# Kernel tuning notes

Hardware: AMD Instinct MI355X
Metric: run time of the kernel (lower is better)

Reference implementation:

```python
import jax, jax.numpy as jnp
import numpy as np

B, C, H, W = 4, 256, 64, 64
CP = C // 4  # embedding_channels, k=4 hardcoded
# branch index -> (key-stream i, query/value-stream j); streams: 0=t,1=b,2=m
IIDX = np.array([0, 0, 0, 1, 1, 1, 2, 2, 2])  # which stream feeds k
JIDX = np.array([0, 1, 2, 0, 1, 2, 0, 1, 2])  # which stream feeds q and v


def setup_inputs() -> dict:
    key = jax.random.key(0)
    ks = jax.random.split(key, 6)
    scale = 0.05
    return {
        "t": jax.random.normal(ks[0], (B, C, H, W), jnp.float32),
        "b": jax.random.normal(ks[1], (B, C, H, W), jnp.float32),
        "m": jax.random.normal(ks[2], (B, C, H, W), jnp.float32),
        "W_qkv": jax.random.normal(ks[3], (9, C, C), jnp.float32) * scale,
        "W_red": jax.random.normal(ks[4], (9, CP, C), jnp.float32) * scale,
        "W_rec": jax.random.normal(ks[5], (9, C, CP), jnp.float32) * scale,
    }


def _pool(x):
    # ChannelAttention: global avg pool + global max pool -> [B, C']
    return jnp.mean(x, axis=(2, 3)) + jnp.max(x, axis=(2, 3))


def _channel_attention(q, k, v, w_red, w_rec):
    # q,k,v: [B,C,H,W]; w_red: [C',C]; w_rec: [C,C']
    ori = q + k + v
    red = lambda x: jax.nn.relu(jnp.einsum("bchw,ec->behw", x, w_red))
    qr, kr, vr = red(q), red(k), red(v)
    f = _pool(kr)  # key   -> [B,C']
    g = _pool(qr)  # query -> [B,C']
    h = _pool(vr)  # value -> [B,C']
    # s = f^T g : [B,C',C']; softmax over dim=1 (rows), per torch nn.Softmax(dim=1)
    s = f[:, :, None] * g[:, None, :]
    beta = jax.nn.softmax(s, axis=1)
    vout = jnp.einsum("bi,bij->bj", h, beta)  # [B,C']
    # recovery 1x1 conv on [B,C',1,1]; bilinear upsample from 1x1 == broadcast
    o = jax.nn.sigmoid(jnp.einsum("be,ce->bc", vout, w_rec))  # [B,C]
    return o[:, :, None, None] * ori


def reference(t, b, m, W_qkv, W_red, W_rec):
    x = jnp.stack([t, b, m])  # [3,B,C,H,W]
    Wp = W_qkv.reshape(3, 3, C, C)  # [stream, (q,k,v), C_out, C_in]
    proj = jnp.einsum("sbchw,sjec->sjbehw", x, Wp)  # [3,3,B,C,H,W]
    Q, K, V = proj[:, 0], proj[:, 1], proj[:, 2]  # each [3,B,C,H,W]
    q9, k9, v9 = Q[JIDX], K[IIDX], V[JIDX]  # [9,B,C,H,W]
    outs = jax.vmap(_channel_attention)(q9, k9, v9, W_red, W_rec)
    return outs.sum(axis=0)
```

## Files before the change

### kernel.cpp

```cpp
#include <hip/hip_runtime.h>

#define Bn 4
#define Cn 256
#define HWn 4096
#define CPn 64
#define MP 640

typedef unsigned short u16;
typedef unsigned int u32;

using short8  = __attribute__((ext_vector_type(8))) short;
using floatx4 = __attribute__((ext_vector_type(4))) float;

static __device__ __forceinline__ u16 f2bf(float f) {
    union { float f; u32 u; } v; v.f = f;
    u32 r = (v.u + 0x7FFFu + ((v.u >> 16) & 1u)) >> 16;
    return (u16)r;
}

static __device__ __forceinline__ void gld16(const u16* g, u16* l) {
    __builtin_amdgcn_global_load_lds(
        (const __attribute__((address_space(1))) u32*)g,
        (__attribute__((address_space(3))) u32*)l, 16, 0, 0);
}


__global__ __launch_bounds__(256) void prep(
    const float* __restrict__ Tt, const float* __restrict__ Bt, const float* __restrict__ Mt,
    const float* __restrict__ Wqkv, const float* __restrict__ Wred,
    u16* __restrict__ xT, u16* __restrict__ CWp)
{
    __shared__ u16 T[64][72];
    __shared__ float As[16][64];
    __shared__ float Bs[16][64];
    const int t = threadIdx.x;

    if (blockIdx.z < 3) {
        const int s  = blockIdx.z, b = blockIdx.y;
        const int ct = blockIdx.x & 3, hwt = blockIdx.x >> 2;
        const int c0 = ct * 64, hw0 = hwt * 64;
        const float* X = (s == 0 ? Tt : (s == 1 ? Bt : Mt)) + (size_t)b * Cn * HWn;

        const int cl = t >> 2, q = t & 3;
        const float* src = X + (size_t)(c0 + cl) * HWn + hw0 + q * 16;
        #pragma unroll
        for (int u = 0; u < 4; ++u) {
            const float4 v = *(const float4*)(src + u * 4);
            T[cl][q * 16 + u * 4 + 0] = f2bf(v.x);
            T[cl][q * 16 + u * 4 + 1] = f2bf(v.y);
            T[cl][q * 16 + u * 4 + 2] = f2bf(v.z);
            T[cl][q * 16 + u * 4 + 3] = f2bf(v.w);
        }
        __syncthreads();

        const int wl = t >> 2;
        u16* dst = xT + ((size_t)((s * Bn + b) * HWn) + hw0 + wl) * Cn + c0 + q * 16;
        #pragma unroll
        for (int u = 0; u < 2; ++u) {
            u32 w0 = (u32)T[q * 16 + u * 8 + 0][wl] | ((u32)T[q * 16 + u * 8 + 1][wl] << 16);
            u32 w1 = (u32)T[q * 16 + u * 8 + 2][wl] | ((u32)T[q * 16 + u * 8 + 3][wl] << 16);
            u32 w2 = (u32)T[q * 16 + u * 8 + 4][wl] | ((u32)T[q * 16 + u * 8 + 5][wl] << 16);
            u32 w3 = (u32)T[q * 16 + u * 8 + 6][wl] | ((u32)T[q * 16 + u * 8 + 7][wl] << 16);
            uint4 pk = {w0, w1, w2, w3};
            *(uint4*)(dst + u * 8) = pk;
        }
        return;
    }

    const int lin = blockIdx.y * 256 + blockIdx.x;
    if (lin >= 108) return;
    const int c0  = (lin & 3) * 64;
    const int rest = lin >> 2;
    const int y9 = rest % 9, s = rest / 9;
    const int tt = y9 / 3, m3 = y9 % 3;
    const int idx = (tt == 1) ? (3 * s + m3) : (3 * m3 + s);

    const float* A  = Wred + (size_t)idx * CPn * Cn;
    const float* Bm = Wqkv + (size_t)(3 * s + tt) * Cn * Cn;

    const int ty = t >> 4, tx = t & 15;
    float acc[4][4] = {};

    for (int k0 = 0; k0 < Cn; k0 += 16) {
        {
            const int r = t >> 2, eq = (t & 3) * 4;
            const float4 a = *(const float4*)(A + (size_t)r * Cn + k0 + eq);
            As[eq + 0][r] = a.x; As[eq + 1][r] = a.y; As[eq + 2][r] = a.z; As[eq + 3][r] = a.w;
        }
        {
            const int r = t >> 4, cq = (t & 15) * 4;
            *(float4*)(&Bs[r][cq]) = *(const float4*)(Bm + (size_t)(k0 + r) * Cn + c0 + cq);
        }
        __syncthreads();
        #pragma unroll
        for (int k = 0; k < 16; ++k) {
            const float4 a4 = *(const float4*)(&As[k][ty * 4]);
            const float4 b4 = *(const float4*)(&Bs[k][tx * 4]);
            const float a[4] = {a4.x, a4.y, a4.z, a4.w};
            const float bb[4] = {b4.x, b4.y, b4.z, b4.w};
            #pragma unroll
            for (int i = 0; i < 4; ++i)
                #pragma unroll
                for (int j = 0; j < 4; ++j)
                    acc[i][j] = fmaf(a[i], bb[j], acc[i][j]);
        }
        __syncthreads();
    }

    u16* outp = CWp + (size_t)s * MP * Cn;
    #pragma unroll
    for (int i = 0; i < 4; ++i) {
        const int row = tt * 192 + m3 * 64 + ty * 4 + i;
        unsigned long long pk =
            (unsigned long long)f2bf(acc[i][0]) |
            ((unsigned long long)f2bf(acc[i][1]) << 16) |
            ((unsigned long long)f2bf(acc[i][2]) << 32) |
            ((unsigned long long)f2bf(acc[i][3]) << 48);
        *(unsigned long long*)(outp + (size_t)row * Cn + c0 + tx * 4) = pk;
    }
}

#define NSUB 16

__global__ __launch_bounds__(256, 1) void redpool_mfma(
    const u16* __restrict__ xT, const u16* __restrict__ CWp,
    float* __restrict__ Psum, float* __restrict__ Pmax)
{
    const int s   = blockIdx.z;
    const int mt  = blockIdx.x >> 4, nch = blockIdx.x & 15;
    const int m0  = mt * 128;
    const int nbase = nch * 1024;

    const u16* Ap = CWp + (size_t)s * MP * Cn;
    const u16* Bp = xT + (size_t)s * Bn * HWn * Cn;

    __shared__ __align__(16) u16 Bs[2][32 * 512];

    const int t = threadIdx.x;
    const int w = t >> 6, lane = t & 63;
    const int l15 = lane & 15, q = lane >> 4;
    const int wr = w >> 1, wc = w & 1;

    short8 af[4][8];
    {
        const u16* Arow = Ap + (size_t)(m0 + wr * 64 + l15) * Cn + q * 8;
        #pragma unroll
        for (int i = 0; i < 4; ++i)
            #pragma unroll
            for (int kk = 0; kk < 8; ++kk)
                af[i][kk] = *(const short8*)(Arow + (size_t)(i * 16) * Cn + kk * 32);
    }

    auto stageB = [&](int it, int buf) {
        const u16* Bsrc = Bp + (size_t)(nbase + it * 64 + l15) * Cn + q * 8;
        #pragma unroll
        for (int pi = 0; pi < 8; ++pi) {
            const int p = w * 8 + pi;
            gld16(Bsrc + (size_t)((p >> 3) * 16) * Cn + (p & 7) * 32, &Bs[buf][p * 512]);
        }
    };
    stageB(0, 0);

    float rs[4][4] = {};
    float rm[4][4] = {};

    for (int it = 0; it < NSUB; ++it) {
        __syncthreads();
        if (it + 1 < NSUB) stageB(it + 1, (it + 1) & 1);
        const u16* bb = Bs[it & 1];

        floatx4 acc[4][2] = {};
        #pragma unroll
        for (int kk = 0; kk < 8; ++kk) {
            short8 bf[2];
            #pragma unroll
            for (int j = 0; j < 2; ++j)
                bf[j] = *(const short8*)&bb[((wc * 2 + j) * 8 + kk) * 512 + lane * 8];
            #pragma unroll
            for (int i = 0; i < 4; ++i)
                #pragma unroll
                for (int j = 0; j < 2; ++j)
                    acc[i][j] = __builtin_amdgcn_mfma_f32_16x16x32_bf16(af[i][kk], bf[j], acc[i][j], 0, 0, 0);
        }
        #pragma unroll
        for (int i = 0; i < 4; ++i)
            #pragma unroll
            for (int r = 0; r < 4; ++r) {
                const float v0 = fmaxf(acc[i][0][r], 0.f);
                const float v1 = fmaxf(acc[i][1][r], 0.f);
                rs[i][r] += v0 + v1;
                rm[i][r] = fmaxf(rm[i][r], fmaxf(v0, v1));
            }
    }

    #pragma unroll
    for (int i = 0; i < 4; ++i)
        #pragma unroll
        for (int r = 0; r < 4; ++r) {
            #pragma unroll
            for (int off = 1; off < 16; off <<= 1) {
                rs[i][r] += __shfl_xor(rs[i][r], off);
                rm[i][r] = fmaxf(rm[i][r], __shfl_xor(rm[i][r], off));
            }
        }

    __syncthreads();
    float* Lsum = (float*)&Bs[0][0];
    float* Lmax = Lsum + 256;
    if (l15 == 0) {
        #pragma unroll
        for (int i = 0; i < 4; ++i)
            #pragma unroll
            for (int r = 0; r < 4; ++r) {
                const int row = wr * 64 + i * 16 + q * 4 + r;
                Lsum[wc * 128 + row] = rs[i][r];
                Lmax[wc * 128 + row] = rm[i][r];
            }
    }
    __syncthreads();
    if (t < 128) {
        const int R = m0 + t;
        const size_t o = ((size_t)s * MP + R) * 16 + nch;
        Psum[o] = Lsum[t] + Lsum[128 + t];
        Pmax[o] = fmaxf(Lmax[t], Lmax[128 + t]);
    }
}

__global__ __launch_bounds__(64) void attn_small(
    const float* __restrict__ Psum, const float* __restrict__ Pmax,
    float* __restrict__ vout)
{
    const int idx = blockIdx.x / Bn;
    const int bb  = blockIdx.x % Bn;
    __shared__ float ff[CPn], gg[CPn], hh[CPn];
    const int t = threadIdx.x;

    float v[3];
    #pragma unroll
    for (int tt = 0; tt < 3; ++tt) {
        const int s_ = (tt == 1) ? idx / 3 : idx % 3;
        const int m3 = (tt == 1) ? idx % 3 : idx / 3;
        const int R  = tt * 192 + m3 * 64 + t;
        const size_t base = ((size_t)s_ * MP + R) * 16 + bb * 4;
        float sm = 0.f, mx = 0.f;
        #pragma unroll
        for (int u = 0; u < 4; ++u) {
            sm += Psum[base + u];
            mx = fmaxf(mx, Pmax[base + u]);
        }
        v[tt] = sm * (1.0f / HWn) + mx;
    }
    gg[t] = v[0];
    ff[t] = v[1];
    hh[t] = v[2];
    __syncthreads();

    const float gj = gg[t];
    float mx = -1e30f;
    for (int i = 0; i < CPn; ++i) mx = fmaxf(mx, ff[i] * gj);
    float den = 0.f, num = 0.f;
    for (int i = 0; i < CPn; ++i) {
        const float e = expf(ff[i] * gj - mx);
        den += e;
        num += hh[i] * e;
    }
    vout[((size_t)idx * Bn + bb) * CPn + t] = num / den;
}

__global__ __launch_bounds__(256) void build_M(
    const float* __restrict__ Wqkv, const float* __restrict__ Wrec,
    const float* __restrict__ vout, u16* __restrict__ Mm)
{
    const int s = blockIdx.x >> 8, m = blockIdx.x & 255;
    const int b = blockIdx.y;
    const int t = threadIdx.x;
    __shared__ float cc[2];

    if (t < CPn) {
        float d[6];
        #pragma unroll
        for (int j = 0; j < 6; ++j) {
            const int idx = (j < 3) ? (s + 3 * j) : (3 * s + (j - 3));
            d[j] = vout[((size_t)idx * Bn + b) * CPn + t] *
                   Wrec[((size_t)idx * Cn + m) * CPn + t];
        }
        #pragma unroll
        for (int off = 32; off >= 1; off >>= 1)
            #pragma unroll
            for (int j = 0; j < 6; ++j)
                d[j] += __shfl_xor(d[j], off);
        if (t == 0) {
            float cA = 0.f, cK = 0.f;
            #pragma unroll
            for (int j = 0; j < 3; ++j) {
                cA += 1.0f / (1.0f + expf(-d[j]));
                cK += 1.0f / (1.0f + expf(-d[j + 3]));
            }
            cc[0] = cA; cc[1] = cK;
        }
    }
    __syncthreads();
    const float cA = cc[0], cK = cc[1];
    const float wq = Wqkv[((size_t)(3 * s + 0) * Cn + m) * Cn + t];
    const float wk = Wqkv[((size_t)(3 * s + 1) * Cn + m) * Cn + t];
    const float wv = Wqkv[((size_t)(3 * s + 2) * Cn + m) * Cn + t];
    Mm[((size_t)(b * 256 + m)) * 768 + s * 256 + t] = f2bf(cA * (wq + wv) + cK * wk);
}

__global__ __launch_bounds__(256, 1) void final_mfma(
    const u16* __restrict__ xT, const u16* __restrict__ Mm,
    float* __restrict__ out)
{
    const int b  = blockIdx.y;
    const int mt = blockIdx.x >> 5, nt = blockIdx.x & 31;
    const int m0 = mt * 128, n0 = nt * 128;

    __shared__ __align__(16) u16 As[2][32 * 512];
    __shared__ __align__(16) u16 Bs[2][32 * 512];

    const int t = threadIdx.x;
    const int w = t >> 6, lane = t & 63;
    const int l15 = lane & 15, q = lane >> 4;
    const int rb = (w >> 1) * 64, cb = (w & 1) * 64;

    auto stage = [&](int it, int buf) {
        const int k0 = it * 128;
        const int s = k0 >> 8, c0 = k0 & 255;
        const u16* Asrc = Mm + (size_t)(b * 256 + m0 + l15) * 768 + k0 + q * 8;
        const u16* Bsrc = xT + ((size_t)((s * Bn + b) * HWn) + n0 + l15) * Cn + c0 + q * 8;
        #pragma unroll
        for (int pi = 0; pi < 8; ++pi) {
            const int p = w * 8 + pi;
            const size_t roff = (size_t)((p >> 2) * 16);
            gld16(Asrc + roff * 768 + (p & 3) * 32, &As[buf][p * 512]);
            gld16(Bsrc + roff * Cn + (p & 3) * 32, &Bs[buf][p * 512]);
        }
    };
    stage(0, 0);

    floatx4 acc[4][4] = {};

    for (int it = 0; it < 6; ++it) {
        __syncthreads();
        if (it + 1 < 6) stage(it + 1, (it + 1) & 1);
        const u16* as = As[it & 1];
        const u16* bs = Bs[it & 1];
        #pragma unroll
        for (int kk = 0; kk < 4; ++kk) {
            short8 af[4], bf[4];
            #pragma unroll
            for (int i = 0; i < 4; ++i)
                af[i] = *(const short8*)&as[((((w >> 1) * 4 + i) << 2) + kk) * 512 + lane * 8];
            #pragma unroll
            for (int j = 0; j < 4; ++j)
                bf[j] = *(const short8*)&bs[((((w & 1) * 4 + j) << 2) + kk) * 512 + lane * 8];
            #pragma unroll
            for (int i = 0; i < 4; ++i)
                #pragma unroll
                for (int j = 0; j < 4; ++j)
                    acc[i][j] = __builtin_amdgcn_mfma_f32_16x16x32_bf16(af[i], bf[j], acc[i][j], 0, 0, 0);
        }
    }

    #pragma unroll
    for (int i = 0; i < 4; ++i)
        #pragma unroll
        for (int j = 0; j < 4; ++j)
            #pragma unroll
            for (int r = 0; r < 4; ++r) {
                const int row = m0 + rb + i * 16 + q * 4 + r;
                const int col = n0 + cb + j * 16 + l15;
                out[((size_t)(b * 256) + row) * HWn + col] = acc[i][j][r];
            }
}

extern "C" void kernel_launch(void* const* d_in, const int* in_sizes, int n_in,
                              void* d_out, int out_size, void* d_ws, size_t ws_size,
                              hipStream_t stream)
{
    const float* Tt   = (const float*)d_in[0];
    const float* Bt   = (const float*)d_in[1];
    const float* Mt   = (const float*)d_in[2];
    const float* Wqkv = (const float*)d_in[3];
    const float* Wred = (const float*)d_in[4];
    const float* Wrec = (const float*)d_in[5];
    float* out = (float*)d_out;

    unsigned char* p = (unsigned char*)d_ws;
    u16* xT = (u16*)p;            p += (size_t)3 * Bn * HWn * Cn * 2;
    u16* Mm = (u16*)p;            p += (size_t)Bn * 256 * 768 * 2;
    u16* CWp = (u16*)p;           p += (size_t)3 * MP * Cn * 2;
    float* Psum = (float*)p;      p += (size_t)3 * MP * 16 * 4;
    float* Pmax = (float*)p;      p += (size_t)3 * MP * 16 * 4;
    float* vout = (float*)p;      p += (size_t)9 * Bn * CPn * 4;

    prep        <<<dim3(256, Bn, 4), 256, 0, stream>>>(Tt, Bt, Mt, Wqkv, Wred, xT, CWp);
    redpool_mfma<<<dim3(80, 1, 3),   256, 0, stream>>>(xT, CWp, Psum, Pmax);
    attn_small  <<<9 * Bn,            64, 0, stream>>>(Psum, Pmax, vout);
    build_M     <<<dim3(768, Bn),    256, 0, stream>>>(Wqkv, Wrec, vout, Mm);
    final_mfma  <<<dim3(64, Bn),     256, 0, stream>>>(xT, Mm, out);
}
```

Before: 168.5 us.

## Fuse all stages into one persistent kernel with software grid barriers

Replaces five separate kernel launches with one persistent 256-block kernel. The prep, reduction-pool, attention, M-build and final GEMM phases are separated by atomic-counter grid barriers, and the counters are cleared with a memset beforehand. This removes launch gaps and inter-kernel drain, but limits parallelism to 256 blocks per phase. It also adds spin-wait barrier overhead and s_setprio hints around the MFMA loop, and correctness relies on all blocks being co-resident.

After: 258.9 us. 1.54x slower.

```diff
diff --git a/kernel.cpp b/kernel.cpp
--- a/kernel.cpp
+++ b/kernel.cpp
@@ -8,6 +8,7 @@
 
 typedef unsigned short u16;
 typedef unsigned int u32;
+typedef unsigned long long u64;
 
 using short8  = __attribute__((ext_vector_type(8))) short;
 using floatx4 = __attribute__((ext_vector_type(4))) float;
@@ -24,354 +25,352 @@
         (__attribute__((address_space(3))) u32*)l, 16, 0, 0);
 }
 
-
-__global__ __launch_bounds__(256) void prep(
+__global__ __launch_bounds__(256, 1) void mega(
     const float* __restrict__ Tt, const float* __restrict__ Bt, const float* __restrict__ Mt,
-    const float* __restrict__ Wqkv, const float* __restrict__ Wred,
-    u16* __restrict__ xT, u16* __restrict__ CWp)
+    const float* __restrict__ Wqkv, const float* __restrict__ Wred, const float* __restrict__ Wrec,
+    u16* __restrict__ xT, u16* __restrict__ CWp,
+    float* __restrict__ Psum, float* __restrict__ Pmax,
+    float* __restrict__ vout, u16* __restrict__ Mm,
+    float* __restrict__ out, u32* __restrict__ gcnt)
 {
-    __shared__ u16 T[64][72];
-    __shared__ float As[16][64];
-    __shared__ float Bs[16][64];
-    const int t = threadIdx.x;
-
-    if (blockIdx.z < 3) {
-        const int s  = blockIdx.z, b = blockIdx.y;
-        const int ct = blockIdx.x & 3, hwt = blockIdx.x >> 2;
-        const int c0 = ct * 64, hw0 = hwt * 64;
-        const float* X = (s == 0 ? Tt : (s == 1 ? Bt : Mt)) + (size_t)b * Cn * HWn;
-
-        const int cl = t >> 2, q = t & 3;
-        const float* src = X + (size_t)(c0 + cl) * HWn + hw0 + q * 16;
-        #pragma unroll
-        for (int u = 0; u < 4; ++u) {
-            const float4 v = *(const float4*)(src + u * 4);
-            T[cl][q * 16 + u * 4 + 0] = f2bf(v.x);
-            T[cl][q * 16 + u * 4 + 1] = f2bf(v.y);
-            T[cl][q * 16 + u * 4 + 2] = f2bf(v.z);
-            T[cl][q * 16 + u * 4 + 3] = f2bf(v.w);
-        }
-        __syncthreads();
-
-        const int wl = t >> 2;
-        u16* dst = xT + ((size_t)((s * Bn + b) * HWn) + hw0 + wl) * Cn + c0 + q * 16;
-        #pragma unroll
-        for (int u = 0; u < 2; ++u) {
-            u32 w0 = (u32)T[q * 16 + u * 8 + 0][wl] | ((u32)T[q * 16 + u * 8 + 1][wl] << 16);
-            u32 w1 = (u32)T[q * 16 + u * 8 + 2][wl] | ((u32)T[q * 16 + u * 8 + 3][wl] << 16);
-            u32 w2 = (u32)T[q * 16 + u * 8 + 4][wl] | ((u32)T[q * 16 + u * 8 + 5][wl] << 16);
-            u32 w3 = (u32)T[q * 16 + u * 8 + 6][wl] | ((u32)T[q * 16 + u * 8 + 7][wl] << 16);
-            uint4 pk = {w0, w1, w2, w3};
-            *(uint4*)(dst + u * 8) = pk;
-        }
-        return;
-    }
-
-    const int lin = blockIdx.y * 256 + blockIdx.x;
-    if (lin >= 108) return;
-    const int c0  = (lin & 3) * 64;
-    const int rest = lin >> 2;
-    const int y9 = rest % 9, s = rest / 9;
-    const int tt = y9 / 3, m3 = y9 % 3;
-    const int idx = (tt == 1) ? (3 * s + m3) : (3 * m3 + s);
-
-    const float* A  = Wred + (size_t)idx * CPn * Cn;
-    const float* Bm = Wqkv + (size_t)(3 * s + tt) * Cn * Cn;
-
-    const int ty = t >> 4, tx = t & 15;
-    float acc[4][4] = {};
-
-    for (int k0 = 0; k0 < Cn; k0 += 16) {
-        {
-            const int r = t >> 2, eq = (t & 3) * 4;
-            const float4 a = *(const float4*)(A + (size_t)r * Cn + k0 + eq);
-            As[eq + 0][r] = a.x; As[eq + 1][r] = a.y; As[eq + 2][r] = a.z; As[eq + 3][r] = a.w;
-        }
-        {
-            const int r = t >> 4, cq = (t & 15) * 4;
-            *(float4*)(&Bs[r][cq]) = *(const float4*)(Bm + (size_t)(k0 + r) * Cn + c0 + cq);
-        }
-        __syncthreads();
-        #pragma unroll
-        for (int k = 0; k < 16; ++k) {
-            const float4 a4 = *(const float4*)(&As[k][ty * 4]);
-            const float4 b4 = *(const float4*)(&Bs[k][tx * 4]);
-            const float a[4] = {a4.x, a4.y, a4.z, a4.w};
-            const float bb[4] = {b4.x, b4.y, b4.z, b4.w};
-            #pragma unroll
-            for (int i = 0; i < 4; ++i)
-                #pragma unroll
-                for (int j = 0; j < 4; ++j)
-                    acc[i][j] = fmaf(a[i], bb[j], acc[i][j]);
-        }
-        __syncthreads();
-    }
-
-    u16* outp = CWp + (size_t)s * MP * Cn;
-    #pragma unroll
-    for (int i = 0; i < 4; ++i) {
-        const int row = tt * 192 + m3 * 64 + ty * 4 + i;
-        unsigned long long pk =
-            (unsigned long long)f2bf(acc[i][0]) |
-            ((unsigned long long)f2bf(acc[i][1]) << 16) |
-            ((unsigned long long)f2bf(acc[i][2]) << 32) |
-            ((unsigned long long)f2bf(acc[i][3]) << 48);
-        *(unsigned long long*)(outp + (size_t)row * Cn + c0 + tx * 4) = pk;
-    }
-}
-
-#define NSUB 16
-
-__global__ __launch_bounds__(256, 1) void redpool_mfma(
-    const u16* __restrict__ xT, const u16* __restrict__ CWp,
-    float* __restrict__ Psum, float* __restrict__ Pmax)
-{
-    const int s   = blockIdx.z;
-    const int mt  = blockIdx.x >> 4, nch = blockIdx.x & 15;
-    const int m0  = mt * 128;
-    const int nbase = nch * 1024;
-
-    const u16* Ap = CWp + (size_t)s * MP * Cn;
-    const u16* Bp = xT + (size_t)s * Bn * HWn * Cn;
-
-    __shared__ __align__(16) u16 Bs[2][32 * 512];
-
-    const int t = threadIdx.x;
+    __shared__ __align__(16) u16 SM[65536];
+    const int t   = threadIdx.x;
+    const int blk = blockIdx.x;
     const int w = t >> 6, lane = t & 63;
     const int l15 = lane & 15, q = lane >> 4;
-    const int wr = w >> 1, wc = w & 1;
-
-    short8 af[4][8];
+    const u32 nb = gridDim.x;
+
+    auto gbar = [&](int id) {
+        __syncthreads();
+        if (t == 0) {
+            __threadfence();
+            atomicAdd(&gcnt[id * 16], 1u);
+            int guard = 0;
+            while (atomicAdd(&gcnt[id * 16], 0u) < nb && guard < 20000000) ++guard;
+            __threadfence();
+        }
+        __syncthreads();
+    };
+
     {
-        const u16* Arow = Ap + (size_t)(m0 + wr * 64 + l15) * Cn + q * 8;
+        u16 (*T)[72] = (u16(*)[72])SM;
+        const int cl = t >> 2, qq = t & 3;
+        #pragma unroll 1
+        for (int i = 0; i < 12; ++i) {
+            const int tile = blk * 12 + i;
+            const int hwt = tile & 63, ct = (tile >> 6) & 3;
+            const int b = (tile >> 8) & 3, s = tile >> 10;
+            const int c0 = ct * 64, hw0 = hwt * 64;
+            const float* X = (s == 0 ? Tt : (s == 1 ? Bt : Mt)) + (size_t)b * Cn * HWn;
+            const float* src = X + (size_t)(c0 + cl) * HWn + hw0 + qq * 16;
+            #pragma unroll
+            for (int u = 0; u < 4; ++u) {
+                const float4 v = *(const float4*)(src + u * 4);
+                u64 pk = (u64)f2bf(v.x) | ((u64)f2bf(v.y) << 16) |
+                         ((u64)f2bf(v.z) << 32) | ((u64)f2bf(v.w) << 48);
+                *(u64*)&T[cl][qq * 16 + u * 4] = pk;
+            }
+            __syncthreads();
+            u16* dst = xT + ((size_t)((s * Bn + b) * HWn) + hw0 + cl) * Cn + c0 + qq * 16;
+            #pragma unroll
+            for (int u = 0; u < 2; ++u) {
+                u32 w0 = (u32)T[qq*16+u*8+0][cl] | ((u32)T[qq*16+u*8+1][cl] << 16);
+                u32 w1 = (u32)T[qq*16+u*8+2][cl] | ((u32)T[qq*16+u*8+3][cl] << 16);
+                u32 w2 = (u32)T[qq*16+u*8+4][cl] | ((u32)T[qq*16+u*8+5][cl] << 16);
+                u32 w3 = (u32)T[qq*16+u*8+6][cl] | ((u32)T[qq*16+u*8+7][cl] << 16);
+                uint4 pk4 = {w0, w1, w2, w3};
+                *(uint4*)(dst + u * 8) = pk4;
+            }
+            __syncthreads();
+        }
+
+        if (blk < 108) {
+            float (*As)[64]  = (float(*)[64])SM;
+            float (*Bsc)[64] = (float(*)[64])((char*)SM + 4096);
+            const int c0   = (blk & 3) * 64;
+            const int rest = blk >> 2;
+            const int y9 = rest % 9, s = rest / 9;
+            const int tt = y9 / 3, m3 = y9 % 3;
+            const int idx = (tt == 1) ? (3 * s + m3) : (3 * m3 + s);
+            const float* A  = Wred + (size_t)idx * CPn * Cn;
+            const float* Bm = Wqkv + (size_t)(3 * s + tt) * Cn * Cn;
+            const int ty = t >> 4, tx = t & 15;
+            float acc[4][4] = {};
+            for (int k0 = 0; k0 < Cn; k0 += 16) {
+                {
+                    const int r = t >> 2, eq = (t & 3) * 4;
+                    const float4 a = *(const float4*)(A + (size_t)r * Cn + k0 + eq);
+                    As[eq+0][r]=a.x; As[eq+1][r]=a.y; As[eq+2][r]=a.z; As[eq+3][r]=a.w;
+                }
+                {
+                    const int r = t >> 4, cq = (t & 15) * 4;
+                    *(float4*)(&Bsc[r][cq]) = *(const float4*)(Bm + (size_t)(k0+r)*Cn + c0 + cq);
+                }
+                __syncthreads();
+                #pragma unroll
+                for (int k = 0; k < 16; ++k) {
+                    const float4 a4 = *(const float4*)(&As[k][ty*4]);
+                    const float4 b4 = *(const float4*)(&Bsc[k][tx*4]);
+                    const float a_[4]  = {a4.x, a4.y, a4.z, a4.w};
+                    const float bb_[4] = {b4.x, b4.y, b4.z, b4.w};
+                    #pragma unroll
+                    for (int i2 = 0; i2 < 4; ++i2)
+                        #pragma unroll
+                        for (int j2 = 0; j2 < 4; ++j2)
+                            acc[i2][j2] = fmaf(a_[i2], bb_[j2], acc[i2][j2]);
+                }
+                __syncthreads();
+            }
+            u16* outp = CWp + (size_t)s * MP * Cn;
+            #pragma unroll
+            for (int i2 = 0; i2 < 4; ++i2) {
+                const int row = tt * 192 + m3 * 64 + ty * 4 + i2;
+                u64 pk = (u64)f2bf(acc[i2][0]) | ((u64)f2bf(acc[i2][1]) << 16) |
+                         ((u64)f2bf(acc[i2][2]) << 32) | ((u64)f2bf(acc[i2][3]) << 48);
+                *(u64*)(outp + (size_t)row * Cn + c0 + tx * 4) = pk;
+            }
+        }
+    }
+    gbar(0);
+
+    if (blk < 240) {
+        const int s = blk / 80, r80 = blk % 80;
+        const int mt = r80 >> 4, nch = r80 & 15;
+        const int m0 = mt * 128;
+        const int nbase = nch * 1024;
+        const u16* Ap = CWp + (size_t)s * MP * Cn;
+        const u16* Bp = xT + (size_t)s * Bn * HWn * Cn;
+        const int wr = w >> 1, wc = w & 1;
+
+        short8 af[4][8];
+        {
+            const u16* Arow = Ap + (size_t)(m0 + wr * 64 + l15) * Cn + q * 8;
+            #pragma unroll
+            for (int i = 0; i < 4; ++i)
+                #pragma unroll
+                for (int kk = 0; kk < 8; ++kk)
+                    af[i][kk] = *(const short8*)(Arow + (size_t)(i * 16) * Cn + kk * 32);
+        }
+
+        u16* const LB0 = SM;
+        u16* const LB1 = SM + 16384;
+        auto stageB = [&](int it, u16* dstb) {
+            const u16* Bsrc = Bp + (size_t)(nbase + it * 64 + l15) * Cn + q * 8;
+            #pragma unroll
+            for (int pi = 0; pi < 8; ++pi) {
+                const int p = w * 8 + pi;
+                gld16(Bsrc + (size_t)((p >> 3) * 16) * Cn + (p & 7) * 32, dstb + p * 512);
+            }
+        };
+        stageB(0, LB0);
+
+        float rs[4][4] = {};
+        float rm[4][4] = {};
+
+        for (int it = 0; it < 16; ++it) {
+            __syncthreads();
+            if (it + 1 < 16) stageB(it + 1, ((it + 1) & 1) ? LB1 : LB0);
+            const u16* bb = (it & 1) ? LB1 : LB0;
+
+            floatx4 acc[4][2] = {};
+            __builtin_amdgcn_s_setprio(1);
+            #pragma unroll
+            for (int kk = 0; kk < 8; ++kk) {
+                short8 bf[2];
+                #pragma unroll
+                for (int j = 0; j < 2; ++j)
+                    bf[j] = *(const short8*)&bb[((wc * 2 + j) * 8 + kk) * 512 + lane * 8];
+                #pragma unroll
+                for (int i = 0; i < 4; ++i)
+                    #pragma unroll
+                    for (int j = 0; j < 2; ++j)
+                        acc[i][j] = __builtin_amdgcn_mfma_f32_16x16x32_bf16(af[i][kk], bf[j], acc[i][j], 0, 0, 0);
+            }
+            __builtin_amdgcn_s_setprio(0);
+            #pragma unroll
+            for (int i = 0; i < 4; ++i)
+                #pragma unroll
+                for (int r = 0; r < 4; ++r) {
+                    const float v0 = fmaxf(acc[i][0][r], 0.f);
+                    const float v1 = fmaxf(acc[i][1][r], 0.f);
+                    rs[i][r] += v0 + v1;
+                    rm[i][r] = fmaxf(rm[i][r], fmaxf(v0, v1));
+                }
+        }
+
         #pragma unroll
         for (int i = 0; i < 4; ++i)
             #pragma unroll
-            for (int kk = 0; kk < 8; ++kk)
-                af[i][kk] = *(const short8*)(Arow + (size_t)(i * 16) * Cn + kk * 32);
+            for (int r = 0; r < 4; ++r) {
+                #pragma unroll
+                for (int off = 1; off < 16; off <<= 1) {
+                    rs[i][r] += __shfl_xor(rs[i][r], off);
+                    rm[i][r] = fmaxf(rm[i][r], __shfl_xor(rm[i][r], off));
+                }
+            }
+
+        __syncthreads();
+        float* Lsum = (float*)SM;
+        float* Lmax = Lsum + 256;
+        if (l15 == 0) {
+            #pragma unroll
+            for (int i = 0; i < 4; ++i)
+                #pragma unroll
+                for (int r = 0; r < 4; ++r) {
+                    const int row = wr * 64 + i * 16 + q * 4 + r;
+                    Lsum[wc * 128 + row] = rs[i][r];
+                    Lmax[wc * 128 + row] = rm[i][r];
+                }
+        }
+        __syncthreads();
+        if (t < 128) {
+            const int R = m0 + t;
+            const size_t o = ((size_t)s * MP + R) * 16 + nch;
+            Psum[o] = Lsum[t] + Lsum[128 + t];
+            Pmax[o] = fmaxf(Lmax[t], Lmax[128 + t]);
+        }
     }
-
-    auto stageB = [&](int it, int buf) {
-        const u16* Bsrc = Bp + (size_t)(nbase + it * 64 + l15) * Cn + q * 8;
-        #pragma unroll
-        for (int pi = 0; pi < 8; ++pi) {
-            const int p = w * 8 + pi;
-            gld16(Bsrc + (size_t)((p >> 3) * 16) * Cn + (p & 7) * 32, &Bs[buf][p * 512]);
-        }
-    };
-    stageB(0, 0);
-
-    float rs[4][4] = {};
-    float rm[4][4] = {};
-
-    for (int it = 0; it < NSUB; ++it) {
+    gbar(1);
+
+    if (blk < 36) {
+        float* ff = (float*)SM;
+        float* gg = ff + 64;
+        float* hh = ff + 128;
+        const int idx = blk >> 2, bb2 = blk & 3;
+        if (t < 64) {
+            float v[3];
+            #pragma unroll
+            for (int tt = 0; tt < 3; ++tt) {
+                const int s_ = (tt == 1) ? idx / 3 : idx % 3;
+                const int m3 = (tt == 1) ? idx % 3 : idx / 3;
+                const int R  = tt * 192 + m3 * 64 + t;
+                const size_t base = ((size_t)s_ * MP + R) * 16 + bb2 * 4;
+                float sm = 0.f, mx = 0.f;
+                #pragma unroll
+                for (int u = 0; u < 4; ++u) {
+                    sm += Psum[base + u];
+                    mx = fmaxf(mx, Pmax[base + u]);
+                }
+                v[tt] = sm * (1.0f / HWn) + mx;
+            }
+            gg[t] = v[0];
+            ff[t] = v[1];
+            hh[t] = v[2];
+        }
         __syncthreads();
-        if (it + 1 < NSUB) stageB(it + 1, (it + 1) & 1);
-        const u16* bb = Bs[it & 1];
-
-        floatx4 acc[4][2] = {};
-        #pragma unroll
-        for (int kk = 0; kk < 8; ++kk) {
-            short8 bf[2];
-            #pragma unroll
-            for (int j = 0; j < 2; ++j)
-                bf[j] = *(const short8*)&bb[((wc * 2 + j) * 8 + kk) * 512 + lane * 8];
-            #pragma unroll
-            for (int i = 0; i < 4; ++i)
-                #pragma unroll
-                for (int j = 0; j < 2; ++j)
-                    acc[i][j] = __builtin_amdgcn_mfma_f32_16x16x32_bf16(af[i][kk], bf[j], acc[i][j], 0, 0, 0);
-        }
+        if (t < 64) {
+            const float gj = gg[t];
+            float mx = -1e30f;
+            for (int i = 0; i < CPn; ++i) mx = fmaxf(mx, ff[i] * gj);
+            float den = 0.f, num = 0.f;
+            for (int i = 0; i < CPn; ++i) {
+                const float e = expf(ff[i] * gj - mx);
+                den += e;
+                num += hh[i] * e;
+            }
+            vout[((size_t)idx * Bn + bb2) * CPn + t] = num / den;
+        }
+    }
+    gbar(2);
+
+    {
+        float* cc = (float*)SM;
+        #pragma unroll 1
+        for (int i = 0; i < 12; ++i) {
+            const int unit = blk * 12 + i;
+            const int b = unit & 3, m = (unit >> 2) & 255, s = unit >> 10;
+            if (t < CPn) {
+                float d[6];
+                #pragma unroll
+                for (int j = 0; j < 6; ++j) {
+                    const int idx = (j < 3) ? (s + 3 * j) : (3 * s + (j - 3));
+                    d[j] = vout[((size_t)idx * Bn + b) * CPn + t] *
+                           Wrec[((size_t)idx * Cn + m) * CPn + t];
+                }
+                #pragma unroll
+                for (int off = 32; off >= 1; off >>= 1)
+                    #pragma unroll
+                    for (int j = 0; j < 6; ++j)
+                        d[j] += __shfl_xor(d[j], off);
+                if (t == 0) {
+                    float cA = 0.f, cK = 0.f;
+                    #pragma unroll
+                    for (int j = 0; j < 3; ++j) {
+                        cA += 1.0f / (1.0f + expf(-d[j]));
+                        cK += 1.0f / (1.0f + expf(-d[j + 3]));
+                    }
+                    cc[0] = cA; cc[1] = cK;
+                }
+            }
+            __syncthreads();
+            const float cA = cc[0], cK = cc[1];
+            const float wq = Wqkv[((size_t)(3 * s + 0) * Cn + m) * Cn + t];
+            const float wk = Wqkv[((size_t)(3 * s + 1) * Cn + m) * Cn + t];
+            const float wv = Wqkv[((size_t)(3 * s + 2) * Cn + m) * Cn + t];
+            Mm[((size_t)(b * 256 + m)) * 768 + s * 256 + t] = f2bf(cA * (wq + wv) + cK * wk);
+            __syncthreads();
+        }
+    }
+    gbar(3);
+
+    {
+        const int b  = blk >> 6, rest = blk & 63;
+        const int mt = rest >> 5, nt = rest & 31;
+        const int m0 = mt * 128, n0 = nt * 128;
+        u16* const A0 = SM;
+        u16* const B0 = SM + 32768;
+        const int rb = (w >> 1) * 64, cb = (w & 1) * 64;
+
+        auto stage = [&](int it, int bufofs) {
+            const int k0 = it * 128;
+            const int s = k0 >> 8, c0 = k0 & 255;
+            const u16* Asrc = Mm + (size_t)(b * 256 + m0 + l15) * 768 + k0 + q * 8;
+            const u16* Bsrc = xT + ((size_t)((s * Bn + b) * HWn) + n0 + l15) * Cn + c0 + q * 8;
+            #pragma unroll
+            for (int pi = 0; pi < 8; ++pi) {
+                const int p = w * 8 + pi;
+                const size_t roff = (size_t)((p >> 2) * 16);
+                gld16(Asrc + roff * 768 + (p & 3) * 32, A0 + bufofs + p * 512);
+                gld16(Bsrc + roff * Cn + (p & 3) * 32, B0 + bufofs + p * 512);
+            }
+        };
+        stage(0, 0);
+
+        floatx4 acc[4][4] = {};
+
+        for (int it = 0; it < 6; ++it) {
+            __syncthreads();
+            if (it + 1 < 6) stage(it + 1, ((it + 1) & 1) * 16384);
+            const u16* as = A0 + (it & 1) * 16384;
+            const u16* bs = B0 + (it & 1) * 16384;
+            #pragma unroll
+            for (int kk = 0; kk < 4; ++kk) {
+                short8 af2[4], bf2[4];
+                #pragma unroll
+                for (int i = 0; i < 4; ++i)
+                    af2[i] = *(const short8*)&as[((((w >> 1) * 4 + i) << 2) + kk) * 512 + lane * 8];
+                #pragma unroll
+                for (int j = 0; j < 4; ++j)
+                    bf2[j] = *(const short8*)&bs[((((w & 1) * 4 + j) << 2) + kk) * 512 + lane * 8];
+                #pragma unroll
+                for (int i = 0; i < 4; ++i)
+                    #pragma unroll
+                    for (int j = 0; j < 4; ++j)
+                        acc[i][j] = __builtin_amdgcn_mfma_f32_16x16x32_bf16(af2[i], bf2[j], acc[i][j], 0, 0, 0);
+            }
+        }
+
         #pragma unroll
         for (int i = 0; i < 4; ++i)
             #pragma unroll
-            for (int r = 0; r < 4; ++r) {
-                const float v0 = fmaxf(acc[i][0][r], 0.f);
-                const float v1 = fmaxf(acc[i][1][r], 0.f);
-                rs[i][r] += v0 + v1;
-                rm[i][r] = fmaxf(rm[i][r], fmaxf(v0, v1));
-            }
+            for (int j = 0; j < 4; ++j)
+                #pragma unroll
+                for (int r = 0; r < 4; ++r) {
+                    const int row = m0 + rb + i * 16 + q * 4 + r;
+                    const int col = n0 + cb + j * 16 + l15;
+                    out[((size_t)(b * 256) + row) * HWn + col] = acc[i][j][r];
+                }
     }
-
-    #pragma unroll
-    for (int i = 0; i < 4; ++i)
-        #pragma unroll
-        for (int r = 0; r < 4; ++r) {
-            #pragma unroll
-            for (int off = 1; off < 16; off <<= 1) {
-                rs[i][r] += __shfl_xor(rs[i][r], off);
-                rm[i][r] = fmaxf(rm[i][r], __shfl_xor(rm[i][r], off));
-            }
-        }
-
-    __syncthreads();
-    float* Lsum = (float*)&Bs[0][0];
-    float* Lmax = Lsum + 256;
-    if (l15 == 0) {
-        #pragma unroll
-        for (int i = 0; i < 4; ++i)
-            #pragma unroll
-            for (int r = 0; r < 4; ++r) {
-                const int row = wr * 64 + i * 16 + q * 4 + r;
-                Lsum[wc * 128 + row] = rs[i][r];
-                Lmax[wc * 128 + row] = rm[i][r];
-            }
-    }
-    __syncthreads();
-    if (t < 128) {
-        const int R = m0 + t;
-        const size_t o = ((size_t)s * MP + R) * 16 + nch;
-        Psum[o] = Lsum[t] + Lsum[128 + t];
-        Pmax[o] = fmaxf(Lmax[t], Lmax[128 + t]);
-    }
-}
-
-__global__ __launch_bounds__(64) void attn_small(
-    const float* __restrict__ Psum, const float* __restrict__ Pmax,
-    float* __restrict__ vout)
-{
-    const int idx = blockIdx.x / Bn;
-    const int bb  = blockIdx.x % Bn;
-    __shared__ float ff[CPn], gg[CPn], hh[CPn];
-    const int t = threadIdx.x;
-
-    float v[3];
-    #pragma unroll
-    for (int tt = 0; tt < 3; ++tt) {
-        const int s_ = (tt == 1) ? idx / 3 : idx % 3;
-        const int m3 = (tt == 1) ? idx % 3 : idx / 3;
-        const int R  = tt * 192 + m3 * 64 + t;
-        const size_t base = ((size_t)s_ * MP + R) * 16 + bb * 4;
-        float sm = 0.f, mx = 0.f;
-        #pragma unroll
-        for (int u = 0; u < 4; ++u) {
-            sm += Psum[base + u];
-            mx = fmaxf(mx, Pmax[base + u]);
-        }
-        v[tt] = sm * (1.0f / HWn) + mx;
-    }
-    gg[t] = v[0];
-    ff[t] = v[1];
-    hh[t] = v[2];
-    __syncthreads();
-
-    const float gj = gg[t];
-    float mx = -1e30f;
-    for (int i = 0; i < CPn; ++i) mx = fmaxf(mx, ff[i] * gj);
-    float den = 0.f, num = 0.f;
-    for (int i = 0; i < CPn; ++i) {
-        const float e = expf(ff[i] * gj - mx);
-        den += e;
-        num += hh[i] * e;
-    }
-    vout[((size_t)idx * Bn + bb) * CPn + t] = num / den;
-}
-
-__global__ __launch_bounds__(256) void build_M(
-    const float* __restrict__ Wqkv, const float* __restrict__ Wrec,
-    const float* __restrict__ vout, u16* __restrict__ Mm)
-{
-    const int s = blockIdx.x >> 8, m = blockIdx.x & 255;
-    const int b = blockIdx.y;
-    const int t = threadIdx.x;
-    __shared__ float cc[2];
-
-    if (t < CPn) {
-        float d[6];
-        #pragma unroll
-        for (int j = 0; j < 6; ++j) {
-            const int idx = (j < 3) ? (s + 3 * j) : (3 * s + (j - 3));
-            d[j] = vout[((size_t)idx * Bn + b) * CPn + t] *
-                   Wrec[((size_t)idx * Cn + m) * CPn + t];
-        }
-        #pragma unroll
-        for (int off = 32; off >= 1; off >>= 1)
-            #pragma unroll
-            for (int j = 0; j < 6; ++j)
-                d[j] += __shfl_xor(d[j], off);
-        if (t == 0) {
-            float cA = 0.f, cK = 0.f;
-            #pragma unroll
-            for (int j = 0; j < 3; ++j) {
-                cA += 1.0f / (1.0f + expf(-d[j]));
-                cK += 1.0f / (1.0f + expf(-d[j + 3]));
-            }
-            cc[0] = cA; cc[1] = cK;
-        }
-    }
-    __syncthreads();
-    const float cA = cc[0], cK = cc[1];
-    const float wq = Wqkv[((size_t)(3 * s + 0) * Cn + m) * Cn + t];
-    const float wk = Wqkv[((size_t)(3 * s + 1) * Cn + m) * Cn + t];
-    const float wv = Wqkv[((size_t)(3 * s + 2) * Cn + m) * Cn + t];
-    Mm[((size_t)(b * 256 + m)) * 768 + s * 256 + t] = f2bf(cA * (wq + wv) + cK * wk);
-}
-
-__global__ __launch_bounds__(256, 1) void final_mfma(
-    const u16* __restrict__ xT, const u16* __restrict__ Mm,
-    float* __restrict__ out)
-{
-    const int b  = blockIdx.y;
-    const int mt = blockIdx.x >> 5, nt = blockIdx.x & 31;
-    const int m0 = mt * 128, n0 = nt * 128;
-
-    __shared__ __align__(16) u16 As[2][32 * 512];
-    __shared__ __align__(16) u16 Bs[2][32 * 512];
-
-    const int t = threadIdx.x;
-    const int w = t >> 6, lane = t & 63;
-    const int l15 = lane & 15, q = lane >> 4;
-    const int rb = (w >> 1) * 64, cb = (w & 1) * 64;
-
-    auto stage = [&](int it, int buf) {
-        const int k0 = it * 128;
-        const int s = k0 >> 8, c0 = k0 & 255;
-        const u16* Asrc = Mm + (size_t)(b * 256 + m0 + l15) * 768 + k0 + q * 8;
-        const u16* Bsrc = xT + ((size_t)((s * Bn + b) * HWn) + n0 + l15) * Cn + c0 + q * 8;
-        #pragma unroll
-        for (int pi = 0; pi < 8; ++pi) {
-            const int p = w * 8 + pi;
-            const size_t roff = (size_t)((p >> 2) * 16);
-            gld16(Asrc + roff * 768 + (p & 3) * 32, &As[buf][p * 512]);
-            gld16(Bsrc + roff * Cn + (p & 3) * 32, &Bs[buf][p * 512]);
-        }
-    };
-    stage(0, 0);
-
-    floatx4 acc[4][4] = {};
-
-    for (int it = 0; it < 6; ++it) {
-        __syncthreads();
-        if (it + 1 < 6) stage(it + 1, (it + 1) & 1);
-        const u16* as = As[it & 1];
-        const u16* bs = Bs[it & 1];
-        #pragma unroll
-        for (int kk = 0; kk < 4; ++kk) {
-            short8 af[4], bf[4];
-            #pragma unroll
-            for (int i = 0; i < 4; ++i)
-                af[i] = *(const short8*)&as[((((w >> 1) * 4 + i) << 2) + kk) * 512 + lane * 8];
-            #pragma unroll
-            for (int j = 0; j < 4; ++j)
-                bf[j] = *(const short8*)&bs[((((w & 1) * 4 + j) << 2) + kk) * 512 + lane * 8];
-            #pragma unroll
-            for (int i = 0; i < 4; ++i)
-                #pragma unroll
-                for (int j = 0; j < 4; ++j)
-                    acc[i][j] = __builtin_amdgcn_mfma_f32_16x16x32_bf16(af[i], bf[j], acc[i][j], 0, 0, 0);
-        }
-    }
-
-    #pragma unroll
-    for (int i = 0; i < 4; ++i)
-        #pragma unroll
-        for (int j = 0; j < 4; ++j)
-            #pragma unroll
-            for (int r = 0; r < 4; ++r) {
-                const int row = m0 + rb + i * 16 + q * 4 + r;
-                const int col = n0 + cb + j * 16 + l15;
-                out[((size_t)(b * 256) + row) * HWn + col] = acc[i][j][r];
-            }
 }
 
 extern "C" void kernel_launch(void* const* d_in, const int* in_sizes, int n_in,
@@ -393,10 +392,9 @@
     float* Psum = (float*)p;      p += (size_t)3 * MP * 16 * 4;
     float* Pmax = (float*)p;      p += (size_t)3 * MP * 16 * 4;
     float* vout = (float*)p;      p += (size_t)9 * Bn * CPn * 4;
-
-    prep        <<<dim3(256, Bn, 4), 256, 0, stream>>>(Tt, Bt, Mt, Wqkv, Wred, xT, CWp);
-    redpool_mfma<<<dim3(80, 1, 3),   256, 0, stream>>>(xT, CWp, Psum, Pmax);
-    attn_small  <<<9 * Bn,            64, 0, stream>>>(Psum, Pmax, vout);
-    build_M     <<<dim3(768, Bn),    256, 0, stream>>>(Wqkv, Wrec, vout, Mm);
-    final_mfma  <<<dim3(64, Bn),     256, 0, stream>>>(xT, Mm, out);
+    u32* gcnt = (u32*)p;          p += 256;
+
+    hipMemsetAsync(gcnt, 0, 256, stream);
+    mega<<<dim3(256), dim3(256), 0, stream>>>(Tt, Bt, Mt, Wqkv, Wred, Wrec,
+                                              xT, CWp, Psum, Pmax, vout, Mm, out, gcnt);
 }
```
